# Performance work log

Hardware: AMD Instinct MI355X
Metric: run time of the kernel (lower is better)

The kernel has to match this reference:

```python
import jax, jax.numpy as jnp
import numpy as np

N_NODES = 50000
N_EDGES = 1600000
D_V, D_E, D_ATTN = 256, 128, 128


def setup_inputs() -> dict:
    key = jax.random.key(0)
    ks = jax.random.split(key, 10)
    scale = 0.05
    nodes = jax.random.normal(ks[0], (N_NODES, D_V), dtype=jnp.float32)
    edges = jax.random.normal(ks[1], (N_EDGES, D_E), dtype=jnp.float32)
    edge_index = jax.random.randint(ks[2], (2, N_EDGES), 0, N_NODES, dtype=jnp.int64 if jax.config.jax_enable_x64 else jnp.int32)
    Wq = jax.random.normal(ks[3], (D_ATTN, D_V), dtype=jnp.float32) * scale
    bq = jnp.zeros((D_ATTN,), dtype=jnp.float32)
    Wk = jax.random.normal(ks[4], (D_ATTN, D_V), dtype=jnp.float32) * scale
    bk = jnp.zeros((D_ATTN,), dtype=jnp.float32)
    Wv = jax.random.normal(ks[5], (D_ATTN, D_E), dtype=jnp.float32) * scale
    bv = jnp.zeros((D_ATTN,), dtype=jnp.float32)
    return {"nodes": nodes, "edges": edges, "edge_index": edge_index,
            "Wq": Wq, "bq": bq, "Wk": Wk, "bk": bk, "Wv": Wv, "bv": bv}


def reference(nodes, edges, edge_index, Wq, bq, Wk, bk, Wv, bv):
    # nodes: [N, d_v], edges: [E, d_e], edge_index: [2, E] (s=sender, r=receiver)
    s, r = edge_index[0], edge_index[1]
    lrelu = jax.nn.leaky_relu  # default negative_slope=0.01, matches torch F.leaky_relu
    q = lrelu(nodes @ Wq.T + bq)      # [N, d_attn]
    k = lrelu(nodes[s] @ Wk.T + bk)   # [E, d_attn]  (key of sender node per edge)
    v = lrelu(edges @ Wv.T + bv)      # [E, d_attn]
    d = q.shape[-1]
    # Per-edge logit = <q[r[e]], k[e]> / sqrt(d).  Masked dense softmax over the
    # [N, E] score matrix with mask (r[e]==i) is exactly a segment softmax by receiver.
    logits = jnp.sum(q[r] * k, axis=-1) / jnp.sqrt(jnp.asarray(d, q.dtype))  # [E]
    N = nodes.shape[0]
    m = jax.ops.segment_max(logits, r, num_segments=N)          # [N]
    p = jnp.exp(logits - m[r])                                  # [E]
    denom = jax.ops.segment_sum(p, r, num_segments=N)           # [N]
    attn = p / denom[r]                                         # [E]
    out = jax.ops.segment_sum(attn[:, None] * v, r, num_segments=N)  # [N, d_attn]
    return out
```

## Files before the change

kernel.cpp:

```cpp
#include <hip/hip_runtime.h>
#include <hip/hip_bf16.h>
#include <cstdint>

#define NN 50000
#define NE 1600000
#define DV 256
#define DA 128

using floatx4 = __attribute__((ext_vector_type(4))) float;
using shortx8 = __attribute__((ext_vector_type(8))) short;

__device__ __forceinline__ unsigned short f2bf(float f) {
    union { float f; uint32_t u; } v; v.f = f;
    uint32_t u = v.u;
    uint32_t r = (u + 0x7FFFu + ((u >> 16) & 1u)) >> 16;
    return (unsigned short)r;
}
__device__ __forceinline__ float bflo(uint32_t u) {
    union { uint32_t u; float f; } v; v.u = u << 16; return v.f;
}
__device__ __forceinline__ float bfhi(uint32_t u) {
    union { uint32_t u; float f; } v; v.u = u & 0xFFFF0000u; return v.f;
}
__device__ __forceinline__ shortx8 pack8(float4 a, float4 b) {
    shortx8 u;
    u[0] = (short)f2bf(a.x); u[1] = (short)f2bf(a.y);
    u[2] = (short)f2bf(a.z); u[3] = (short)f2bf(a.w);
    u[4] = (short)f2bf(b.x); u[5] = (short)f2bf(b.y);
    u[6] = (short)f2bf(b.z); u[7] = (short)f2bf(b.w);
    return u;
}

__global__ void init_zero(float4* __restrict__ out, float4* __restrict__ denom,
                          float4* __restrict__ cnt) {
    const float4 z = make_float4(0.f, 0.f, 0.f, 0.f);
    int i = blockIdx.x * blockDim.x + threadIdx.x;
    const int stride = gridDim.x * blockDim.x;
    for (int j = i; j < NN * 128 / 4; j += stride) out[j] = z;
    if (i < NN / 4) { denom[i] = z; cnt[i] = z; }
}

__global__ void cast_w_kernel(const float* __restrict__ wq, const float* __restrict__ wk,
                              const float* __restrict__ wv, unsigned short* __restrict__ out) {
    int i = blockIdx.x * blockDim.x + threadIdx.x;
    if (i < 32768)       out[i] = f2bf(wq[i]);
    else if (i < 65536)  out[i] = f2bf(wk[i - 32768]);
    else if (i < 81920)  out[i] = f2bf(wv[i - 65536]);
}

__global__ void hist_kernel(const int* __restrict__ ridx, int* __restrict__ cnt) {
    int e = blockIdx.x * blockDim.x + threadIdx.x;
    if (e < NE) atomicAdd(&cnt[ridx[e]], 1);
}

__global__ __launch_bounds__(1024)
void scan_kernel(const int* __restrict__ cnt, int* __restrict__ offs) {
    __shared__ int part[1024];
    const int tid = threadIdx.x;
    const int PER = (NN + 1023) / 1024;
    int base = tid * PER;
    int s = 0;
    for (int i = 0; i < PER; ++i) { int idx = base + i; if (idx < NN) s += cnt[idx]; }
    part[tid] = s;
    __syncthreads();
    for (int off = 1; off < 1024; off <<= 1) {
        int v = (tid >= off) ? part[tid - off] : 0;
        __syncthreads();
        part[tid] += v;
        __syncthreads();
    }
    int excl = (tid == 0) ? 0 : part[tid - 1];
    for (int i = 0; i < PER; ++i) {
        int idx = base + i;
        if (idx < NN) { offs[idx] = excl; excl += cnt[idx]; }
    }
}

__global__ void scatter_kernel(const int* __restrict__ ridx, int* __restrict__ offs,
                               int* __restrict__ perm) {
    int e = blockIdx.x * blockDim.x + threadIdx.x;
    if (e >= NE) return;
    int r = ridx[e];
    int pos = atomicAdd(&offs[r], 1);
    perm[pos] = e;
}

__global__ __launch_bounds__(256)
void proj_qk(const float* __restrict__ A, const unsigned short* __restrict__ Wst,
             const float* __restrict__ bq, const float* __restrict__ bk,
             unsigned short* __restrict__ qbf, unsigned short* __restrict__ kbf, int M) {
    __shared__ unsigned short Al[64 * 32];
    __shared__ unsigned short Bl[256 * 32];
    const int tid = threadIdx.x;
    const int lane = tid & 63, w = tid >> 6;
    const int m0 = blockIdx.x * 64;
    constexpr int K = 256;

    floatx4 acc[16];
#pragma unroll
    for (int i = 0; i < 16; ++i) acc[i] = (floatx4)0.0f;

    for (int kk = 0; kk < K; kk += 32) {
#pragma unroll
        for (int it = 0; it < 2; ++it) {
            int j = tid + it * 256;
            int row = j >> 3;
            int c4 = (j & 7) * 4;
            float4 f = make_float4(0.f, 0.f, 0.f, 0.f);
            int gm = m0 + row;
            if (gm < M) f = *reinterpret_cast<const float4*>(A + (size_t)gm * K + kk + c4);
            ushort4 u; u.x = f2bf(f.x); u.y = f2bf(f.y); u.z = f2bf(f.z); u.w = f2bf(f.w);
            *reinterpret_cast<ushort4*>(&Al[row * 32 + c4]) = u;
        }
#pragma unroll
        for (int it = 0; it < 4; ++it) {
            int j = tid + it * 256;
            int row = j >> 2;
            int c8 = (j & 3) * 8;
            uint4 v = *reinterpret_cast<const uint4*>(Wst + (size_t)row * K + kk + c8);
            *reinterpret_cast<uint4*>(&Bl[row * 32 + c8]) = v;
        }
        __syncthreads();
        shortx8 af = *reinterpret_cast<const shortx8*>(&Al[(w * 16 + (lane & 15)) * 32 + 8 * (lane >> 4)]);
#pragma unroll
        for (int nt = 0; nt < 16; ++nt) {
            shortx8 bf = *reinterpret_cast<const shortx8*>(&Bl[(nt * 16 + (lane & 15)) * 32 + 8 * (lane >> 4)]);
            acc[nt] = __builtin_amdgcn_mfma_f32_16x16x32_bf16(af, bf, acc[nt], 0, 0, 0);
        }
        __syncthreads();
    }
    const int col = lane & 15;
    const int rbase = m0 + w * 16 + 4 * (lane >> 4);
#pragma unroll
    for (int nt = 0; nt < 16; ++nt) {
        int gn = nt * 16 + col;
        bool isq = gn < 128;
        int oc = isq ? gn : gn - 128;
        float b = isq ? bq[oc] : bk[oc];
        unsigned short* O = isq ? qbf : kbf;
#pragma unroll
        for (int reg = 0; reg < 4; ++reg) {
            int gm = rbase + reg;
            if (gm < M) {
                float v = acc[nt][reg] + b;
                v = v > 0.f ? v : 0.01f * v;
                O[(size_t)gm * 128 + oc] = f2bf(v);
            }
        }
    }
}

__global__ __launch_bounds__(512)
void v_gemm_fused(const float* __restrict__ Ed, const unsigned short* __restrict__ wv_bf,
                  const float* __restrict__ bv,
                  const unsigned short* __restrict__ qbf, const unsigned short* __restrict__ kbf,
                  const int* __restrict__ sidx, const int* __restrict__ ridx,
                  const int* __restrict__ perm,
                  float* __restrict__ out, float* __restrict__ denom) {
    __shared__ __align__(16) char smem[51264];
    unsigned short* Bf = reinterpret_cast<unsigned short*>(smem);
    unsigned short* Vl = reinterpret_cast<unsigned short*>(smem);
    int*   rs_local = reinterpret_cast<int*>(smem + 49152);
    float* pl       = reinterpret_cast<float*>(smem + 49664);
    int*   segstart = reinterpret_cast<int*>(smem + 50176);
    int*   segnode  = reinterpret_cast<int*>(smem + 50688);
    unsigned long long* masks = reinterpret_cast<unsigned long long*>(smem + 51200);
    int* nseg_s = reinterpret_cast<int*>(smem + 51216);

    const int tid = threadIdx.x;
    const int lane = tid & 63, w = tid >> 6;
    const size_t m0 = (size_t)blockIdx.x * 128;

    const int erow = tid >> 2;
    const int qt = tid & 3;
    const int e_id = perm[m0 + erow];
    const int sN = sidx[e_id];
    const int rN = ridx[e_id];
    if (qt == 0) rs_local[erow] = rN;

    {
        const uint4* kp = reinterpret_cast<const uint4*>(kbf + (size_t)sN * 128 + qt * 32);
        const uint4* qp = reinterpret_cast<const uint4*>(qbf + (size_t)rN * 128 + qt * 32);
        float acq = 0.f;
#pragma unroll
        for (int i = 0; i < 4; ++i) {
            uint4 qa = qp[i], ka = kp[i];
            acq += bflo(qa.x) * bflo(ka.x) + bfhi(qa.x) * bfhi(ka.x);
            acq += bflo(qa.y) * bflo(ka.y) + bfhi(qa.y) * bfhi(ka.y);
            acq += bflo(qa.z) * bflo(ka.z) + bfhi(qa.z) * bfhi(ka.z);
            acq += bflo(qa.w) * bflo(ka.w) + bfhi(qa.w) * bfhi(ka.w);
        }
        acq += __shfl_xor(acq, 1);
        acq += __shfl_xor(acq, 2);
        if (qt == 0) pl[erow] = __expf(acq * 0.08838834764831845f);
    }

#pragma unroll
    for (int it = 0; it < 4; ++it) {
        int s = tid + it * 512;
        int g = s >> 6, l = s & 63;
        int kt4 = g >> 3, nt = g & 7;
        uint4 v = *reinterpret_cast<const uint4*>(
            wv_bf + (size_t)(nt * 16 + (l & 15)) * 128 + kt4 * 32 + 8 * (l >> 4));
        *reinterpret_cast<uint4*>(smem + s * 16) = v;
    }

    const float* arow = Ed + (size_t)e_id * 128;
    const int cst = (tid & 3) * 8;
    const int chunkp = (tid & 3) ^ ((tid >> 3) & 3);
    {
        float4 fa = *reinterpret_cast<const float4*>(arow + cst);
        float4 fb = *reinterpret_cast<const float4*>(arow + cst + 4);
        shortx8 u = pack8(fa, fb);
        *reinterpret_cast<shortx8*>(smem + 32768 + erow * 64 + chunkp * 16) = u;
    }
    __syncthreads();

    if (tid < 128) {
        bool flag = (tid == 0) || (rs_local[tid] != rs_local[tid - 1]);
        unsigned long long mk = __ballot(flag);
        if (lane == 0) masks[w] = mk;
    }
    __syncthreads();
    if (tid < 128) {
        bool flag = (tid == 0) || (rs_local[tid] != rs_local[tid - 1]);
        unsigned long long mk0 = masks[0], mk1 = masks[1];
        if (tid == 0) *nseg_s = __popcll(mk0) + __popcll(mk1);
        if (flag) {
            int rank = (tid < 64)
                ? __popcll(mk0 & ((1ull << tid) - 1ull))
                : __popcll(mk0) + ((tid == 64) ? 0 : __popcll(mk1 & ((1ull << (tid - 64)) - 1ull)));
            segstart[rank] = tid;
            segnode[rank] = rs_local[tid];
        }
    }

    floatx4 acc[8];
#pragma unroll
    for (int i = 0; i < 8; ++i) acc[i] = (floatx4)0.0f;
    const int afr_off = (w * 16 + (lane & 15)) * 64 +
                        (((lane >> 4) ^ (((lane & 15) >> 1) & 3)) << 4);
#pragma unroll
    for (int kt = 0; kt < 4; ++kt) {
        const int rbase = (kt & 1) ? 40960 : 32768;
        const int wbase = (kt & 1) ? 32768 : 40960;
        float4 fa, fb;
        if (kt < 3) {
            fa = *reinterpret_cast<const float4*>(arow + (kt + 1) * 32 + cst);
            fb = *reinterpret_cast<const float4*>(arow + (kt + 1) * 32 + cst + 4);
        }
        shortx8 af = *reinterpret_cast<const shortx8*>(smem + rbase + afr_off);
#pragma unroll
        for (int nt = 0; nt < 8; ++nt) {
            shortx8 bfr = *reinterpret_cast<const shortx8*>(smem + (((kt * 8 + nt) * 64 + lane) << 4));
            acc[nt] = __builtin_amdgcn_mfma_f32_16x16x32_bf16(af, bfr, acc[nt], 0, 0, 0);
        }
        if (kt < 3) {
            shortx8 u = pack8(fa, fb);
            *reinterpret_cast<shortx8*>(smem + wbase + erow * 64 + chunkp * 16) = u;
        }
        __syncthreads();
    }

    const int colb = lane & 15;
    const int rquad = w * 16 + 4 * (lane >> 4);
    float pe[4];
#pragma unroll
    for (int reg = 0; reg < 4; ++reg) pe[reg] = pl[rquad + reg];
#pragma unroll
    for (int nt = 0; nt < 8; ++nt) {
        float b = bv[nt * 16 + colb];
#pragma unroll
        for (int reg = 0; reg < 4; ++reg) {
            float v = acc[nt][reg] + b;
            v = v > 0.f ? v : 0.01f * v;
            Vl[(rquad + reg) * 128 + nt * 16 + colb] = f2bf(v * pe[reg]);
        }
    }
    __syncthreads();

    const int colc = tid & 127;
    const int sg = tid >> 7;
    const int ns = *nseg_s;
    for (int s2 = sg; s2 < ns; s2 += 4) {
        int a = segstart[s2];
        int bnd = (s2 + 1 < ns) ? segstart[s2 + 1] : 128;
        float sum = 0.f;
        for (int rr = a; rr < bnd; ++rr) sum += bflo((uint32_t)Vl[rr * 128 + colc]);
        int node = segnode[s2];
        bool interior = (s2 > 0) && (s2 + 1 < ns);
        if (interior) out[(size_t)node * 128 + colc] = sum;
        else          atomicAdd(&out[(size_t)node * 128 + colc], sum);
        if (colc == 0) {
            float ds = 0.f;
            for (int rr = a; rr < bnd; ++rr) ds += pl[rr];
            if (interior) denom[node] = ds;
            else          atomicAdd(&denom[node], ds);
        }
    }
}

__global__ void normalize_kernel(float* __restrict__ out, const float* __restrict__ denom) {
    int i = blockIdx.x * blockDim.x + threadIdx.x;
    if (i >= NN * 128 / 4) return;
    int node = (i * 4) >> 7;
    float d = denom[node];
    float inv = d > 0.f ? 1.0f / d : 0.f;
    float4* o = reinterpret_cast<float4*>(out) + i;
    float4 v = *o;
    v.x *= inv; v.y *= inv; v.z *= inv; v.w *= inv;
    *o = v;
}

extern "C" void kernel_launch(void* const* d_in, const int* in_sizes, int n_in,
                              void* d_out, int out_size, void* d_ws, size_t ws_size,
                              hipStream_t stream) {
    const float* nodes = (const float*)d_in[0];
    const float* edges = (const float*)d_in[1];
    const int*   eidx  = (const int*)d_in[2];
    const float* Wq = (const float*)d_in[3];
    const float* bq = (const float*)d_in[4];
    const float* Wk = (const float*)d_in[5];
    const float* bk = (const float*)d_in[6];
    const float* Wv = (const float*)d_in[7];
    const float* bv = (const float*)d_in[8];
    const int* sidx = eidx;
    const int* ridx = eidx + NE;

    char* ws = (char*)d_ws;
    unsigned short* wq_bf = (unsigned short*)ws;
    unsigned short* wv_bf = wq_bf + 65536;
    unsigned short* q_bf  = (unsigned short*)(ws + 163840);
    unsigned short* k_bf  = q_bf + (size_t)NN * 128;
    char* ws2 = ws + 163840 + 2 * (size_t)NN * 128 * 2;
    float* denom = (float*)ws2;
    int*   cnt   = (int*)(denom + NN);
    int*   offs  = cnt + NN;
    int*   perm  = offs + NN;
    float* out = (float*)d_out;

    init_zero<<<2048, 256, 0, stream>>>((float4*)out, (float4*)denom, (float4*)cnt);
    cast_w_kernel<<<320, 256, 0, stream>>>(Wq, Wk, Wv, wq_bf);
    hist_kernel<<<(NE + 255) / 256, 256, 0, stream>>>(ridx, cnt);
    scan_kernel<<<1, 1024, 0, stream>>>(cnt, offs);
    scatter_kernel<<<(NE + 255) / 256, 256, 0, stream>>>(ridx, offs, perm);
    proj_qk<<<(NN + 63) / 64, 256, 0, stream>>>(nodes, wq_bf, bq, bk, q_bf, k_bf, NN);
    v_gemm_fused<<<NE / 128, 512, 0, stream>>>(edges, wv_bf, bv, q_bf, k_bf, sidx, ridx,
                                               perm, out, denom);
    normalize_kernel<<<(NN * 128 / 4 + 255) / 256, 256, 0, stream>>>(out, denom);
}
```

Measured before the change: 640.2 us.

## Preload full edge rows into fragment-layout LDS, drop per-k-step syncs, remap blocks per XCD

Each thread now loads its entire 128-float edge row up front, before the q·k dot product, so those global loads overlap with the gathers. The converted bf16 rows are written once into an MFMA-fragment-ordered LDS layout, replacing the double-buffered loop that needed a barrier every k-step. Block indices are remapped so each XCD handles a contiguous range of edge tiles, improving L2 locality. The cost is more LDS (about 66KB) and more registers, which may lower occupancy.

New measurement: 893.2 us. 39.5% more time.

```diff
diff --git a/kernel.cpp b/kernel.cpp
--- a/kernel.cpp
+++ b/kernel.cpp
@@ -157,19 +157,22 @@
                   const int* __restrict__ sidx, const int* __restrict__ ridx,
                   const int* __restrict__ perm,
                   float* __restrict__ out, float* __restrict__ denom) {
-    __shared__ __align__(16) char smem[51264];
-    unsigned short* Bf = reinterpret_cast<unsigned short*>(smem);
+    __shared__ __align__(16) char smem[67616];
     unsigned short* Vl = reinterpret_cast<unsigned short*>(smem);
-    int*   rs_local = reinterpret_cast<int*>(smem + 49152);
-    float* pl       = reinterpret_cast<float*>(smem + 49664);
-    int*   segstart = reinterpret_cast<int*>(smem + 50176);
-    int*   segnode  = reinterpret_cast<int*>(smem + 50688);
-    unsigned long long* masks = reinterpret_cast<unsigned long long*>(smem + 51200);
-    int* nseg_s = reinterpret_cast<int*>(smem + 51216);
+    int*   rs_local = reinterpret_cast<int*>(smem + 65536);
+    float* pl       = reinterpret_cast<float*>(smem + 66048);
+    int*   segstart = reinterpret_cast<int*>(smem + 66560);
+    int*   segnode  = reinterpret_cast<int*>(smem + 67072);
+    unsigned long long* masks = reinterpret_cast<unsigned long long*>(smem + 67584);
+    int* nseg_s = reinterpret_cast<int*>(smem + 67600);
 
     const int tid = threadIdx.x;
     const int lane = tid & 63, w = tid >> 6;
-    const size_t m0 = (size_t)blockIdx.x * 128;
+
+    const int bid = blockIdx.x;
+    const int xcd = bid & 7;
+    const int nbid = ((xcd < 4) ? xcd * 1563 : 4 * 1563 + (xcd - 4) * 1562) + (bid >> 3);
+    const size_t m0 = (size_t)nbid * 128;
 
     const int erow = tid >> 2;
     const int qt = tid & 3;
@@ -177,6 +180,14 @@
     const int sN = sidx[e_id];
     const int rN = ridx[e_id];
     if (qt == 0) rs_local[erow] = rN;
+
+    const float* arow = Ed + (size_t)e_id * 128;
+    float4 fa[4], fb[4];
+#pragma unroll
+    for (int ks = 0; ks < 4; ++ks) {
+        fa[ks] = *reinterpret_cast<const float4*>(arow + qt * 32 + ks * 8);
+        fb[ks] = *reinterpret_cast<const float4*>(arow + qt * 32 + ks * 8 + 4);
+    }
 
     {
         const uint4* kp = reinterpret_cast<const uint4*>(kbf + (size_t)sN * 128 + qt * 32);
@@ -205,14 +216,11 @@
         *reinterpret_cast<uint4*>(smem + s * 16) = v;
     }
 
-    const float* arow = Ed + (size_t)e_id * 128;
-    const int cst = (tid & 3) * 8;
-    const int chunkp = (tid & 3) ^ ((tid >> 3) & 3);
     {
-        float4 fa = *reinterpret_cast<const float4*>(arow + cst);
-        float4 fb = *reinterpret_cast<const float4*>(arow + cst + 4);
-        shortx8 u = pack8(fa, fb);
-        *reinterpret_cast<shortx8*>(smem + 32768 + erow * 64 + chunkp * 16) = u;
+        const int fragbase = 32768 + (((erow >> 4) * 4 + qt) << 10) + ((erow & 15) << 4);
+#pragma unroll
+        for (int ks = 0; ks < 4; ++ks)
+            *reinterpret_cast<shortx8*>(smem + fragbase + ks * 256) = pack8(fa[ks], fb[ks]);
     }
     __syncthreads();
 
@@ -238,29 +246,17 @@
     floatx4 acc[8];
 #pragma unroll
     for (int i = 0; i < 8; ++i) acc[i] = (floatx4)0.0f;
-    const int afr_off = (w * 16 + (lane & 15)) * 64 +
-                        (((lane >> 4) ^ (((lane & 15) >> 1) & 3)) << 4);
 #pragma unroll
     for (int kt = 0; kt < 4; ++kt) {
-        const int rbase = (kt & 1) ? 40960 : 32768;
-        const int wbase = (kt & 1) ? 32768 : 40960;
-        float4 fa, fb;
-        if (kt < 3) {
-            fa = *reinterpret_cast<const float4*>(arow + (kt + 1) * 32 + cst);
-            fb = *reinterpret_cast<const float4*>(arow + (kt + 1) * 32 + cst + 4);
-        }
-        shortx8 af = *reinterpret_cast<const shortx8*>(smem + rbase + afr_off);
+        shortx8 af = *reinterpret_cast<const shortx8*>(
+            smem + 32768 + ((w * 4 + kt) << 10) + (lane << 4));
 #pragma unroll
         for (int nt = 0; nt < 8; ++nt) {
             shortx8 bfr = *reinterpret_cast<const shortx8*>(smem + (((kt * 8 + nt) * 64 + lane) << 4));
             acc[nt] = __builtin_amdgcn_mfma_f32_16x16x32_bf16(af, bfr, acc[nt], 0, 0, 0);
         }
-        if (kt < 3) {
-            shortx8 u = pack8(fa, fb);
-            *reinterpret_cast<shortx8*>(smem + wbase + erow * 64 + chunkp * 16) = u;
-        }
-        __syncthreads();
-    }
+    }
+    __syncthreads();
 
     const int colb = lane & 15;
     const int rquad = w * 16 + 4 * (lane >> 4);
```
